# Kernel optimization log

Measured on AMD Instinct MI355X. Metric: run time of the kernel, lower is better.

Reference implementation:

```python
import jax, jax.numpy as jnp
import numpy as np
from jax import lax

FH, FW = 38, 63          # feature map H,W (600x1000 image, stride 16)
A = 9                    # anchors per location (3 scales x 3 ratios)
POOL = 7                 # cfg.POOLING_SIZE
PRE_NMS, POST_NMS = 6000, 300
NMS_THRESH = 0.7
IM_H, IM_W = 600.0, 1000.0
STRIDE = 16.0


def _make_anchors(h, w, stride=16):
    ratios = np.array([0.5, 1.0, 2.0]); scales = np.array([8.0, 16.0, 32.0])
    base = 16.0; ctr = (base - 1.0) / 2.0
    ws = np.round(np.sqrt(base * base / ratios)); hs = np.round(ws * ratios)
    ws = (ws[:, None] * scales[None, :]).ravel(); hs = (hs[:, None] * scales[None, :]).ravel()
    ba = np.stack([ctr - 0.5 * (ws - 1), ctr - 0.5 * (hs - 1),
                   ctr + 0.5 * (ws - 1), ctr + 0.5 * (hs - 1)], 1)
    sx, sy = np.meshgrid(np.arange(w) * stride, np.arange(h) * stride)
    shifts = np.stack([sx.ravel(), sy.ravel(), sx.ravel(), sy.ravel()], 1)
    return (shifts[:, None, :] + ba[None]).reshape(-1, 4).astype(np.float32)


def _conv(x, w, b, pad):
    y = lax.conv_general_dilated(x, w, (1, 1), pad,
                                 dimension_numbers=('NCHW', 'OIHW', 'NCHW'))
    return y + b[None, :, None, None]


def _bbox_transform_inv(anchors, deltas):
    w = anchors[:, 2] - anchors[:, 0] + 1.0
    h = anchors[:, 3] - anchors[:, 1] + 1.0
    cx = anchors[:, 0] + 0.5 * w
    cy = anchors[:, 1] + 0.5 * h
    dx, dy, dw, dh = deltas[:, 0], deltas[:, 1], deltas[:, 2], deltas[:, 3]
    pcx = dx * w + cx; pcy = dy * h + cy
    pw = jnp.exp(dw) * w; ph = jnp.exp(dh) * h
    return jnp.stack([pcx - 0.5 * pw, pcy - 0.5 * ph,
                      pcx + 0.5 * pw, pcy + 0.5 * ph], 1)


def _nms_keep(boxes, thresh):
    # greedy NMS over score-sorted boxes, fixed-size keep mask
    x1, y1, x2, y2 = boxes[:, 0], boxes[:, 1], boxes[:, 2], boxes[:, 3]
    areas = (x2 - x1 + 1.0) * (y2 - y1 + 1.0)
    iw = jnp.maximum(jnp.minimum(x2[:, None], x2[None, :])
                     - jnp.maximum(x1[:, None], x1[None, :]) + 1.0, 0.0)
    ih = jnp.maximum(jnp.minimum(y2[:, None], y2[None, :])
                     - jnp.maximum(y1[:, None], y1[None, :]) + 1.0, 0.0)
    inter = iw * ih
    iou = inter / (areas[:, None] + areas[None, :] - inter)
    n = boxes.shape[0]; ar = jnp.arange(n)
    def body(i, keep):
        sup = (iou[i] > thresh) & (ar > i) & keep[i]
        return keep & ~sup
    return lax.fori_loop(0, n, body, jnp.ones((n,), bool))


def _crop_and_resize(feat, boxes, crop):
    # feat [C,H,W]; boxes [R,4] normalized (y1,x1,y2,x2); TF crop_and_resize semantics
    C, H, W = feat.shape
    t = jnp.arange(crop, dtype=feat.dtype) / (crop - 1)
    def one(box):
        by1, bx1, by2, bx2 = box
        ys = by1 * (H - 1) + t * (by2 - by1) * (H - 1)
        xs = bx1 * (W - 1) + t * (bx2 - bx1) * (W - 1)
        y0f = jnp.floor(ys); x0f = jnp.floor(xs)
        wy = (ys - y0f)[None, :, None]; wx = (xs - x0f)[None, None, :]
        y0 = jnp.clip(y0f, 0, H - 1).astype(jnp.int32)
        y1i = jnp.clip(y0f + 1, 0, H - 1).astype(jnp.int32)
        x0 = jnp.clip(x0f, 0, W - 1).astype(jnp.int32)
        x1i = jnp.clip(x0f + 1, 0, W - 1).astype(jnp.int32)
        f00 = feat[:, y0][:, :, x0]; f01 = feat[:, y0][:, :, x1i]
        f10 = feat[:, y1i][:, :, x0]; f11 = feat[:, y1i][:, :, x1i]
        return (f00 * (1 - wy) * (1 - wx) + f01 * (1 - wy) * wx
                + f10 * wy * (1 - wx) + f11 * wy * wx)
    return jax.vmap(one)(boxes)


def _forward(net_conv, w_rpn, b_rpn, w_cls, b_cls, w_bbox, b_bbox, anchors):
    # _region_proposal: 3x3 rpn conv + relu, 1x1 cls / bbox heads
    rpn = jax.nn.relu(_conv(net_conv, w_rpn, b_rpn, 'SAME'))
    cls = _conv(rpn, w_cls, b_cls, 'VALID')    # [1,2A,H,W]
    bbox = _conv(rpn, w_bbox, b_bbox, 'VALID')  # [1,4A,H,W]
    # view(1,2,-1,W) softmax: channel a pairs with channel a+A (bg/fg)
    bg, fg = cls[:, :A], cls[:, A:]
    fg_prob = jax.nn.softmax(jnp.stack([bg, fg], axis=1), axis=1)[:, 1]  # [1,A,H,W]
    scores = jnp.transpose(fg_prob, (0, 2, 3, 1)).reshape(-1)            # (H*W*A,)
    deltas = jnp.transpose(bbox, (0, 2, 3, 1)).reshape(-1, 4)
    proposals = _bbox_transform_inv(anchors, deltas)
    proposals = jnp.stack([jnp.clip(proposals[:, 0], 0.0, IM_W - 1.0),
                           jnp.clip(proposals[:, 1], 0.0, IM_H - 1.0),
                           jnp.clip(proposals[:, 2], 0.0, IM_W - 1.0),
                           jnp.clip(proposals[:, 3], 0.0, IM_H - 1.0)], 1)
    # proposal selection is non-differentiable (rois.detach() in original)
    scores_sg = lax.stop_gradient(scores)
    props_sg = lax.stop_gradient(proposals)
    _, order = lax.top_k(scores_sg, PRE_NMS)
    boxes = props_sg[order]
    keep = _nms_keep(boxes, NMS_THRESH)
    idx = jnp.sort(jnp.where(keep, jnp.arange(PRE_NMS), PRE_NMS))[:POST_NMS]
    rois = boxes[jnp.minimum(idx, PRE_NMS - 1)]  # [300,4] (x1,y1,x2,y2)
    # _crop_pool_layer with max_pool=True: crop to 14x14 then 2x2 max pool
    H, W = net_conv.shape[2], net_conv.shape[3]
    x1 = rois[:, 0] / STRIDE; y1 = rois[:, 1] / STRIDE
    x2 = rois[:, 2] / STRIDE; y2 = rois[:, 3] / STRIDE
    norm = jnp.stack([y1 / (H - 1), x1 / (W - 1), y2 / (H - 1), x2 / (W - 1)], 1)
    crops = _crop_and_resize(net_conv[0], norm, 2 * POOL)  # [300,C,14,14]
    R, C = crops.shape[0], crops.shape[1]
    return crops.reshape(R, C, POOL, 2, POOL, 2).max(axis=(3, 5))  # [300,C,7,7]


def setup_inputs():
    key = jax.random.key(0)
    ks = jax.random.split(key, 4)
    net_conv = jax.random.normal(ks[0], (1, 512, FH, FW), jnp.float32)
    w_rpn = jax.random.normal(ks[1], (512, 512, 3, 3), jnp.float32) * 0.01
    b_rpn = jnp.zeros((512,), jnp.float32)
    w_cls = jax.random.normal(ks[2], (2 * A, 512, 1, 1), jnp.float32) * 0.01
    b_cls = jnp.zeros((2 * A,), jnp.float32)
    w_bbox = jax.random.normal(ks[3], (4 * A, 512, 1, 1), jnp.float32) * 0.01
    b_bbox = jnp.zeros((4 * A,), jnp.float32)
    anchors = jnp.asarray(_make_anchors(FH, FW))
    return {"net_conv": net_conv, "w_rpn": w_rpn, "b_rpn": b_rpn,
            "w_cls": w_cls, "b_cls": b_cls, "w_bbox": w_bbox,
            "b_bbox": b_bbox, "anchors": anchors}


def reference(net_conv, w_rpn, b_rpn, w_cls, b_cls, w_bbox, b_bbox, anchors):
    return _forward(net_conv, w_rpn, b_rpn, w_cls, b_cls, w_bbox, b_bbox, anchors)
```

## Files before the change

kernel.cpp:

```cpp
#include <hip/hip_runtime.h>
#include <stdint.h>

#define NPOS 2394
#define CIN 512
#define KK 4608
#define NANCH 21546
#define PRE 6000
#define POST 300
#define NWORD 94
#define NQ 8
#define QLEN 2694
#define FEATT_BYTES 4902912

#define OFF_BH    0
#define OFF_BL    4718592
#define OFF_P0    9437184
#define OFF_SBOX  9437184
#define OFF_KEEP  9533440
#define OFF_DIAG  9633792
#define OFF_P1    14340096
#define OFF_KEYS  19243008
#define OFF_PROP  19415552
#define OFF_RPART 19760384
#define OFF_FPH   20450048
#define OFF_FPL   23179264

typedef _Float16 half8 __attribute__((ext_vector_type(8)));
typedef float f32x4 __attribute__((ext_vector_type(4)));

__device__ __forceinline__ void gload16(const void* g, void* l) {
    __builtin_amdgcn_global_load_lds((const __attribute__((address_space(1))) void*)g,
                                     (__attribute__((address_space(3))) void*)l, 16, 0, 0);
}

__device__ __forceinline__ unsigned long long rl64(unsigned long long v, int l) {
    union { unsigned long long q; unsigned int d[2]; } s; s.q = v;
    unsigned int lo = __builtin_amdgcn_readlane(s.d[0], l);
    unsigned int hi = __builtin_amdgcn_readlane(s.d[1], l);
    return ((unsigned long long)hi << 32) | (unsigned long long)lo;
}

__global__ __launch_bounds__(256) void k_transpose_feat(const float* __restrict__ in,
                                                        float* __restrict__ featT) {
    __shared__ float tl[32][33];
    int tx = threadIdx.x & 31, tg = threadIdx.x >> 5;
    int posBase = blockIdx.x * 32, ciBase = blockIdx.y * 32;
#pragma unroll
    for (int j = 0; j < 4; ++j) {
        int ci = ciBase + tg + j * 8;
        int pos = posBase + tx;
        tl[tg + j * 8][tx] = (pos < NPOS) ? in[(size_t)ci * NPOS + pos] : 0.f;
    }
    __syncthreads();
#pragma unroll
    for (int j = 0; j < 4; ++j) {
        int pos = posBase + tg + j * 8;
        int ci = ciBase + tx;
        if (pos < NPOS) featT[(size_t)pos * 512 + ci] = tl[tx][tg + j * 8];
    }
}

__global__ void k_pad_split(const float* __restrict__ featT,
                            _Float16* __restrict__ FPH, _Float16* __restrict__ FPL) {
    int idx = blockIdx.x * 256 + threadIdx.x;
    int ci = idx & 511;
    int rc = idx >> 9;
    int hp = rc / 65, wp = rc - hp * 65;
    int h = hp - 1, w = wp - 1;
    float a = 0.f;
    if ((unsigned)h < 38u && (unsigned)w < 63u)
        a = featT[(size_t)(h * 63 + w) * 512 + ci] * 16.f;
    _Float16 ah = (_Float16)a;
    _Float16 al = (_Float16)(a - (float)ah);
    FPH[idx] = ah; FPL[idx] = al;
}

__global__ void k_prep_wf16(const float* __restrict__ w,
                            _Float16* __restrict__ BH, _Float16* __restrict__ BL) {
    int idx = blockIdx.x * 256 + threadIdx.x;
    int co = idx / KK;
    int rem = idx - co * KK;
    int p = rem >> 9;
    int ci = rem & 511;
    float b = w[(co * CIN + ci) * 9 + p] * 128.f;
    _Float16 bh = (_Float16)b;
    _Float16 bl = (_Float16)(b - (float)bh);
    BH[idx] = bh; BL[idx] = bl;
}

__global__ __launch_bounds__(256, 3) void k_conv3_mfma(
    const _Float16* __restrict__ FPH, const _Float16* __restrict__ FPL,
    const _Float16* __restrict__ BHp, const _Float16* __restrict__ BLp,
    float* __restrict__ P0, float* __restrict__ P1)
{
    __shared__ __align__(16) char lds[49152];
    const int t = threadIdx.x;
    const int wave = t >> 6, lane = t & 63;
    const int posBase = blockIdx.x * 128;
    const int coBase  = blockIdx.y * 64;
    const int z = blockIdx.z;
    float* __restrict__ P = z ? P1 : P0;
    const int wm = wave >> 1, wn = wave & 1;
    const int lr = lane & 15, lg = lane >> 4;

    int addrA[4][2], addrB[2][2];
#pragma unroll
    for (int m = 0; m < 4; ++m) {
        int row = wm * 64 + m * 16 + lr;
        int x = row & 7;
        addrA[m][0] = row * 128 + ((lg ^ x) << 4);
        addrA[m][1] = row * 128 + (((4 + lg) ^ x) << 4);
    }
#pragma unroll
    for (int n = 0; n < 2; ++n) {
        int row = wn * 32 + n * 16 + lr;
        int x = row & 7;
        addrB[n][0] = 32768 + row * 128 + ((lg ^ x) << 4);
        addrB[n][1] = 32768 + row * 128 + (((4 + lg) ^ x) << 4);
    }

    int baseA[4], ldsAo[4];
#pragma unroll
    for (int s = 0; s < 4; ++s) {
        int row = (wave * 4 + s) * 8 + (lane >> 3);
        int pos = posBase + row;
        int h = pos / 63;
        int w = pos - h * 63;
        int swz = ((lane & 7) ^ (row & 7)) * 8;
        baseA[s] = (h * 65 + w) * 512 + swz;
        ldsAo[s] = (wave * 4 + s) * 1024 + lane * 16;
    }
    int baseB[2], ldsBo[2];
#pragma unroll
    for (int s = 0; s < 2; ++s) {
        int row = (wave * 2 + s) * 8 + (lane >> 3);
        int swz = ((lane & 7) ^ (row & 7)) * 8;
        baseB[s] = (coBase + row) * KK + swz;
        ldsBo[s] = 32768 + (wave * 2 + s) * 1024 + lane * 16;
    }

    f32x4 acc[4][2];
#pragma unroll
    for (int m = 0; m < 4; ++m)
#pragma unroll
        for (int n = 0; n < 2; ++n) acc[m][n] = (f32x4){0.f, 0.f, 0.f, 0.f};

    const int kbeg = z * 2304;
    for (int step = 0; step < 36; ++step) {
        int k0 = kbeg + step * 64;
        int p = k0 >> 9;
        int ci0 = k0 & 511;
        int kh = p / 3;
        int kw = p - kh * 3;
        int dA = (kh * 65 + kw) * 512 + ci0;
#pragma unroll
        for (int s = 0; s < 4; ++s) {
            int so = baseA[s] + dA;
            gload16(FPH + so, lds + ldsAo[s]);
            gload16(FPL + so, lds + 16384 + ldsAo[s]);
        }
#pragma unroll
        for (int s = 0; s < 2; ++s) {
            int so = baseB[s] + k0;
            gload16(BHp + so, lds + ldsBo[s]);
            gload16(BLp + so, lds + 8192 + ldsBo[s]);
        }
        __syncthreads();
#pragma unroll
        for (int ks = 0; ks < 2; ++ks) {
            half8 aH[4], aL[4], bH[2], bL[2];
#pragma unroll
            for (int m = 0; m < 4; ++m) {
                aH[m] = *(const half8*)(lds + addrA[m][ks]);
                aL[m] = *(const half8*)(lds + 16384 + addrA[m][ks]);
            }
#pragma unroll
            for (int n = 0; n < 2; ++n) {
                bH[n] = *(const half8*)(lds + addrB[n][ks]);
                bL[n] = *(const half8*)(lds + 8192 + addrB[n][ks]);
            }
#pragma unroll
            for (int m = 0; m < 4; ++m)
#pragma unroll
                for (int n = 0; n < 2; ++n) {
                    acc[m][n] = __builtin_amdgcn_mfma_f32_16x16x32_f16(aH[m], bH[n], acc[m][n], 0, 0, 0);
                    acc[m][n] = __builtin_amdgcn_mfma_f32_16x16x32_f16(aH[m], bL[n], acc[m][n], 0, 0, 0);
                    acc[m][n] = __builtin_amdgcn_mfma_f32_16x16x32_f16(aL[m], bH[n], acc[m][n], 0, 0, 0);
                }
        }
        __syncthreads();
    }

#pragma unroll
    for (int m = 0; m < 4; ++m) {
        int pbase = posBase + wm * 64 + m * 16 + lg * 4;
        int co = coBase + wn * 32 + lr;
#pragma unroll
        for (int r = 0; r < 4; ++r) {
            int pos = pbase + r;
            if (pos < NPOS) {
                P[(size_t)pos * 512 + co]      = acc[m][0][r] * (1.f / 2048.f);
                P[(size_t)pos * 512 + co + 16] = acc[m][1][r] * (1.f / 2048.f);
            }
        }
    }
}

__global__ __launch_bounds__(256) void k_heads(const float* __restrict__ P0,
                                               const float* __restrict__ P1,
                                               const float* __restrict__ brpn,
                                               const float* __restrict__ wcls,
                                               const float* __restrict__ bcls,
                                               const float* __restrict__ wbbox,
                                               const float* __restrict__ bbbox,
                                               const float* __restrict__ anchors,
                                               float* __restrict__ proposals,
                                               unsigned long long* __restrict__ keys) {
    __shared__ float x[512];
    __shared__ float part[54][4];
    __shared__ float logit[54];
    int pos = blockIdx.x;
    int t = threadIdx.x;
    {
        float v0 = P0[(size_t)pos * 512 + t] + P1[(size_t)pos * 512 + t] + brpn[t];
        float v1 = P0[(size_t)pos * 512 + t + 256] + P1[(size_t)pos * 512 + t + 256] + brpn[t + 256];
        x[t] = v0 > 0.f ? v0 : 0.f;
        x[t + 256] = v1 > 0.f ? v1 : 0.f;
    }
    __syncthreads();
    if (t < 216) {
        int o = t >> 2, q = t & 3;
        const float* wr = (o < 18) ? (wcls + o * 512) : (wbbox + (o - 18) * 512);
        float s = 0.f;
        int base = q * 128;
#pragma unroll 4
        for (int k2 = 0; k2 < 128; ++k2) s += x[base + k2] * wr[base + k2];
        part[o][q] = s;
    }
    __syncthreads();
    if (t < 54) {
        float b = (t < 18) ? bcls[t] : bbbox[t - 18];
        logit[t] = part[t][0] + part[t][1] + part[t][2] + part[t][3] + b;
    }
    __syncthreads();
    if (t < 9) {
        int a = t;
        float bg = logit[a], fg = logit[9 + a];
        float score = 1.f / (1.f + expf(bg - fg));
        float dx = logit[18 + 4 * a], dy = logit[19 + 4 * a];
        float dw = logit[20 + 4 * a], dh = logit[21 + 4 * a];
        int idx = pos * 9 + a;
        float ax1 = anchors[idx * 4 + 0], ay1 = anchors[idx * 4 + 1];
        float ax2 = anchors[idx * 4 + 2], ay2 = anchors[idx * 4 + 3];
        float aw = ax2 - ax1 + 1.f, ah = ay2 - ay1 + 1.f;
        float cx = ax1 + 0.5f * aw, cy = ay1 + 0.5f * ah;
        float pcx = dx * aw + cx, pcy = dy * ah + cy;
        float pw = expf(dw) * aw, ph = expf(dh) * ah;
        float x1 = fminf(fmaxf(pcx - 0.5f * pw, 0.f), 999.f);
        float y1 = fminf(fmaxf(pcy - 0.5f * ph, 0.f), 599.f);
        float x2 = fminf(fmaxf(pcx + 0.5f * pw, 0.f), 999.f);
        float y2 = fminf(fmaxf(pcy + 0.5f * ph, 0.f), 599.f);
        proposals[idx * 4 + 0] = x1; proposals[idx * 4 + 1] = y1;
        proposals[idx * 4 + 2] = x2; proposals[idx * 4 + 3] = y2;
        union { float f; unsigned int i; } sv; sv.f = score;
        keys[idx] = (((unsigned long long)sv.i) << 32) |
                    (unsigned long long)(0xFFFFFFFFu - (unsigned)idx);
    }
}

__global__ __launch_bounds__(256) void k_rank_partial(const unsigned long long* __restrict__ keys,
                                                      unsigned int* __restrict__ rpart) {
    __shared__ unsigned long long kc[1024];
    int i = blockIdx.x * 256 + threadIdx.x;
    int q = blockIdx.y;
    unsigned long long myk = (i < NANCH) ? keys[i] : 0xFFFFFFFFFFFFFFFFull;
    int j0 = q * QLEN;
    int j1 = j0 + QLEN; if (j1 > NANCH) j1 = NANCH;
    unsigned int cnt = 0;
    for (int base = j0; base < j1; base += 1024) {
        int nload = j1 - base; if (nload > 1024) nload = 1024;
        __syncthreads();
        for (int u = threadIdx.x; u < 1024; u += 256)
            kc[u] = (base + u < j1) ? keys[base + u] : 0ull;
        __syncthreads();
        for (int u = 0; u < nload; ++u)
            cnt += (kc[u] > myk) ? 1u : 0u;
    }
    if (i < NANCH) rpart[i * NQ + q] = cnt;
}

__global__ void k_zero_sboxes(float* __restrict__ sboxes) {
    int i = blockIdx.x * 256 + threadIdx.x;
    if (i < PRE * 4) sboxes[i] = 0.f;
}

__global__ void k_rank_scatter(const unsigned int* __restrict__ rpart,
                               const float* __restrict__ proposals,
                               float* __restrict__ sboxes) {
    int i = blockIdx.x * 256 + threadIdx.x;
    if (i >= NANCH) return;
    unsigned int r = 0;
#pragma unroll
    for (int q = 0; q < NQ; q++) r += rpart[i * NQ + q];
    if (r < PRE) {
        sboxes[r * 4 + 0] = proposals[i * 4 + 0];
        sboxes[r * 4 + 1] = proposals[i * 4 + 1];
        sboxes[r * 4 + 2] = proposals[i * 4 + 2];
        sboxes[r * 4 + 3] = proposals[i * 4 + 3];
    }
}

__global__ __launch_bounds__(64) void k_nms_mask(const float* __restrict__ sboxes,
                                                 unsigned long long* __restrict__ mask,
                                                 unsigned long long* __restrict__ diag2) {
    __shared__ float bx[64][4];
    int ib = blockIdx.x, jb = blockIdx.y;
    int lane = threadIdx.x;
    int j = jb * 64 + lane;
    if (j < PRE) {
        bx[lane][0] = sboxes[j * 4 + 0]; bx[lane][1] = sboxes[j * 4 + 1];
        bx[lane][2] = sboxes[j * 4 + 2]; bx[lane][3] = sboxes[j * 4 + 3];
    } else {
        bx[lane][0] = 3e8f; bx[lane][1] = 3e8f; bx[lane][2] = 3e8f; bx[lane][3] = 3e8f;
    }
    __syncthreads();
    int i = ib * 64 + lane;
    if (i >= PRE) return;
    float x1 = sboxes[i * 4 + 0], y1 = sboxes[i * 4 + 1];
    float x2 = sboxes[i * 4 + 2], y2 = sboxes[i * 4 + 3];
    float ar = (x2 - x1 + 1.f) * (y2 - y1 + 1.f);
    unsigned long long bits = 0;
#pragma unroll 4
    for (int u = 0; u < 64; u++) {
        int j2 = jb * 64 + u;
        float iw = fminf(x2, bx[u][2]) - fmaxf(x1, bx[u][0]) + 1.f;
        float ih = fminf(y2, bx[u][3]) - fmaxf(y1, bx[u][1]) + 1.f;
        iw = fmaxf(iw, 0.f); ih = fmaxf(ih, 0.f);
        float inter = iw * ih;
        float arj = (bx[u][2] - bx[u][0] + 1.f) * (bx[u][3] - bx[u][1] + 1.f);
        float iou = inter / (ar + arj - inter);
        if (iou > 0.7f && j2 > i) bits |= (1ull << u);
    }
    mask[(size_t)i * NWORD + jb] = bits;
    if ((ib >> 1) == (jb >> 1)) diag2[(size_t)i * 2 + (jb & 1)] = bits;
}

#define NSLOT 12
__global__ __launch_bounds__(64) void k_nms_scan(const unsigned long long* __restrict__ mask,
                                                 const unsigned long long* __restrict__ diag2,
                                                 int* __restrict__ keep) {
    __shared__ __align__(16) unsigned long long ldsd[12032];
    __shared__ __align__(16) char ldsrow[NSLOT * 1024];
    __shared__ int ldsk[POST];
    const int lane = threadIdx.x;

    {
        const char* g = (const char*)diag2;
        char* l = (char*)ldsd;
        for (int r = 0; r < 94; ++r)
            gload16(g + (size_t)r * 1024 + (size_t)lane * 16, l + r * 1024);
        asm volatile("s_waitcnt vmcnt(0)" ::: "memory");
        __builtin_amdgcn_sched_barrier(0);
    }

    unsigned long long rem0 = 0, rem1 = 0;
    int nk = 0;
    int npend = 0;

    for (int sb = 0; sb < 47; ++sb) {
        if (npend) {
            asm volatile("s_waitcnt vmcnt(0)" ::: "memory");
            __builtin_amdgcn_sched_barrier(0);
            for (int q = 0; q < npend; ++q) {
                const unsigned long long* lr = (const unsigned long long*)(ldsrow + q * 1024);
                rem0 |= lr[lane];
                if (lane < NWORD - 64) rem1 |= lr[64 + lane];
            }
            npend = 0;
        }
        const int w0 = 2 * sb;
        const int base = sb * 128;
        ulonglong2 lo = *reinterpret_cast<const ulonglong2*>(&ldsd[(size_t)(base + lane) * 2]);
        unsigned long long c1b = ldsd[(size_t)(base + 64 + lane) * 2 + 1];

        unsigned long long rm0 = (w0 < 64) ? rl64(rem0, w0) : rl64(rem1, w0 - 64);
        unsigned long long rm1 = (w0 + 1 < 64) ? rl64(rem0, w0 + 1) : rl64(rem1, w0 + 1 - 64);
        const unsigned long long valid1 = (sb == 46) ? ((1ull << 48) - 1) : ~0ull;
        unsigned long long above0 = ~0ull, above1 = ~0ull;

        for (;;) {
            unsigned long long a0 = ~rm0 & above0;
            if (a0) {
                int u = (int)(__ffsll((long long)a0) - 1);
                if (npend == NSLOT) {
                    asm volatile("s_waitcnt vmcnt(0)" ::: "memory");
                    __builtin_amdgcn_sched_barrier(0);
                    for (int q = 0; q < NSLOT; ++q) {
                        const unsigned long long* lr = (const unsigned long long*)(ldsrow + q * 1024);
                        rem0 |= lr[lane];
                        if (lane < NWORD - 64) rem1 |= lr[64 + lane];
                    }
                    npend = 0;
                }
                gload16((const char*)(mask + (size_t)(base + u) * NWORD) + (size_t)lane * 16,
                        ldsrow + npend * 1024);
                ++npend;
                if (lane == 0) ldsk[nk] = base + u;
                ++nk; if (nk == POST) goto done;
                rm0 |= rl64(lo.x, u);
                rm1 |= rl64(lo.y, u);
                above0 = (u == 63) ? 0ull : (~0ull << (u + 1));
                continue;
            }
            unsigned long long a1 = ~rm1 & valid1 & above1;
            if (a1) {
                int u = (int)(__ffsll((long long)a1) - 1);
                if (npend == NSLOT) {
                    asm volatile("s_waitcnt vmcnt(0)" ::: "memory");
                    __builtin_amdgcn_sched_barrier(0);
                    for (int q = 0; q < NSLOT; ++q) {
                        const unsigned long long* lr = (const unsigned long long*)(ldsrow + q * 1024);
                        rem0 |= lr[lane];
                        if (lane < NWORD - 64) rem1 |= lr[64 + lane];
                    }
                    npend = 0;
                }
                gload16((const char*)(mask + (size_t)(base + 64 + u) * NWORD) + (size_t)lane * 16,
                        ldsrow + npend * 1024);
                ++npend;
                if (lane == 0) ldsk[nk] = base + 64 + u;
                ++nk; if (nk == POST) goto done;
                rm1 |= rl64(c1b, u);
                above1 = (u == 63) ? 0ull : (~0ull << (u + 1));
                continue;
            }
            break;
        }
    }
done:
    asm volatile("s_waitcnt vmcnt(0)" ::: "memory");
    for (int k2 = lane; k2 < POST; k2 += 64)
        keep[k2] = (k2 < nk) ? ldsk[k2] : PRE - 1;
}

__global__ __launch_bounds__(256) void k_gather_rois(const float* sboxes, const int* keep,
                                                     float* outF) {
    int t = threadIdx.x;
    float4 box[2];
    int nr = 0;
    for (int r = t; r < POST; r += 256) {
        int ki = keep[r];
        if (ki < 0) ki = 0; if (ki > PRE - 1) ki = PRE - 1;
        box[nr++] = *reinterpret_cast<const float4*>(sboxes + ki * 4);
    }
    __syncthreads();
    nr = 0;
    for (int r = t; r < POST; r += 256) {
        float4 b = box[nr++];
#pragma unroll
        for (int cg = 0; cg < 8; ++cg)
            *reinterpret_cast<float4*>(outF + (size_t)(r * 512 + cg * 64) * 49) = b;
    }
}

__global__ __launch_bounds__(256) void k_crop_fast(const float* __restrict__ featT,
                                                   float* out) {
    __shared__ float lds[4][49 * 65];
    int r = blockIdx.x;
    int w = threadIdx.x >> 6, lane = threadIdx.x & 63;
    int cg = blockIdx.y * 4 + w;
    int c = cg * 64 + lane;
    float* chunk = out + (size_t)(r * 512 + cg * 64) * 49;
    const float4 b = *reinterpret_cast<const float4*>(chunk);
    float x1 = b.x, y1 = b.y, x2 = b.z, y2 = b.w;
    float by1 = (y1 / 16.f) / 37.f, bx1 = (x1 / 16.f) / 62.f;
    float by2 = (y2 / 16.f) / 37.f, bx2 = (x2 / 16.f) / 62.f;
    float dyn = by2 - by1, dxn = bx2 - bx1;
    for (int e = 0; e < 49; ++e) {
        int oy = e / 7, ox = e - oy * 7;
        float vv[4];
#pragma unroll
        for (int dy = 0; dy < 2; ++dy) {
            int sy = 2 * oy + dy;
            float ty = (float)sy / 13.f;
            float ys = by1 * 37.f + (ty * dyn) * 37.f;
            float yf = floorf(ys);
            float wy = ys - yf;
            int y0  = (int)fminf(fmaxf(yf, 0.f), 37.f);
            int y1i = (int)fminf(fmaxf(yf + 1.f, 0.f), 37.f);
#pragma unroll
            for (int dxx = 0; dxx < 2; ++dxx) {
                int sx = 2 * ox + dxx;
                float tx = (float)sx / 13.f;
                float xs = bx1 * 62.f + (tx * dxn) * 62.f;
                float xf = floorf(xs);
                float wx = xs - xf;
                int x0  = (int)fminf(fmaxf(xf, 0.f), 62.f);
                int x1i = (int)fminf(fmaxf(xf + 1.f, 0.f), 62.f);
                float f00 = featT[(size_t)(y0 * 63 + x0) * 512 + c];
                float f01 = featT[(size_t)(y0 * 63 + x1i) * 512 + c];
                float f10 = featT[(size_t)(y1i * 63 + x0) * 512 + c];
                float f11 = featT[(size_t)(y1i * 63 + x1i) * 512 + c];
                vv[dy * 2 + dxx] = f00 * (1.f - wy) * (1.f - wx) + f01 * (1.f - wy) * wx +
                                   f10 * wy * (1.f - wx) + f11 * wy * wx;
            }
        }
        lds[w][e * 65 + lane] = fmaxf(fmaxf(vv[0], vv[1]), fmaxf(vv[2], vv[3]));
    }
    __syncthreads();
    for (int i = lane; i < 64 * 49; i += 64) {
        int cl = i / 49, e = i - cl * 49;
        chunk[i] = lds[w][e * 65 + cl];
    }
}

__global__ __launch_bounds__(64) void k_crop_slow(const float* __restrict__ net,
                                                  float* out) {
    int r = blockIdx.x, cg = blockIdx.y;
    int lane = threadIdx.x;
    int c = cg * 64 + lane;
    const float4 b = *reinterpret_cast<const float4*>(out + (size_t)(r * 512 + cg * 64) * 49);
    float x1 = b.x, y1 = b.y, x2 = b.z, y2 = b.w;
    float by1 = (y1 / 16.f) / 37.f, bx1 = (x1 / 16.f) / 62.f;
    float by2 = (y2 / 16.f) / 37.f, bx2 = (x2 / 16.f) / 62.f;
    float dyn = by2 - by1, dxn = bx2 - bx1;
    const float* fc = net + (size_t)c * NPOS;
    float* orow = out + ((size_t)r * 512 + c) * 49;
    for (int e = 0; e < 49; ++e) {
        int oy = e / 7, ox = e - oy * 7;
        float vv[4];
#pragma unroll
        for (int dy = 0; dy < 2; ++dy) {
            int sy = 2 * oy + dy;
            float ty = (float)sy / 13.f;
            float ys = by1 * 37.f + (ty * dyn) * 37.f;
            float yf = floorf(ys);
            float wy = ys - yf;
            int y0  = (int)fminf(fmaxf(yf, 0.f), 37.f);
            int y1i = (int)fminf(fmaxf(yf + 1.f, 0.f), 37.f);
#pragma unroll
            for (int dxx = 0; dxx < 2; ++dxx) {
                int sx = 2 * ox + dxx;
                float tx = (float)sx / 13.f;
                float xs = bx1 * 62.f + (tx * dxn) * 62.f;
                float xf = floorf(xs);
                float wx = xs - xf;
                int x0  = (int)fminf(fmaxf(xf, 0.f), 62.f);
                int x1i = (int)fminf(fmaxf(xf + 1.f, 0.f), 62.f);
                float f00 = fc[y0 * 63 + x0];
                float f01 = fc[y0 * 63 + x1i];
                float f10 = fc[y1i * 63 + x0];
                float f11 = fc[y1i * 63 + x1i];
                vv[dy * 2 + dxx] = f00 * (1.f - wy) * (1.f - wx) + f01 * (1.f - wy) * wx +
                                   f10 * wy * (1.f - wx) + f11 * wy * wx;
            }
        }
        orow[e] = fmaxf(fmaxf(vv[0], vv[1]), fmaxf(vv[2], vv[3]));
    }
}

extern "C" void kernel_launch(void* const* d_in, const int* in_sizes, int n_in,
                              void* d_out, int out_size, void* d_ws, size_t ws_size,
                              hipStream_t stream) {
    auto find = [&](int count, int fallback) {
        for (int i = 0; i < n_in; ++i) if (in_sizes[i] == count) return i;
        return fallback;
    };
    const float* net   = (const float*)d_in[find(NPOS * CIN, 0)];
    const float* wrpn  = (const float*)d_in[find(512 * KK, 1)];
    const float* brpn  = (const float*)d_in[find(512, 2)];
    const float* wcls  = (const float*)d_in[find(18 * 512, 3)];
    const float* bcls  = (const float*)d_in[find(18, 4)];
    const float* wbbox = (const float*)d_in[find(36 * 512, 5)];
    const float* bbbox = (const float*)d_in[find(36, 6)];
    const float* anch  = (const float*)d_in[find(NANCH * 4, 7)];

    char* ob = (char*)d_out;
    _Float16* BH             = (_Float16*)(ob + OFF_BH);
    _Float16* BL             = (_Float16*)(ob + OFF_BL);
    unsigned long long* mask = (unsigned long long*)(ob + OFF_BH);
    float* P0                = (float*)(ob + OFF_P0);
    float* P1                = (float*)(ob + OFF_P1);
    float* sboxes            = (float*)(ob + OFF_SBOX);
    int* keep                = (int*)(ob + OFF_KEEP);
    unsigned long long* diag2= (unsigned long long*)(ob + OFF_DIAG);
    unsigned long long* keys = (unsigned long long*)(ob + OFF_KEYS);
    float* proposals         = (float*)(ob + OFF_PROP);
    unsigned int* rpart      = (unsigned int*)(ob + OFF_RPART);
    _Float16* FPH            = (_Float16*)(ob + OFF_FPH);
    _Float16* FPL            = (_Float16*)(ob + OFF_FPL);
    float* outF              = (float*)d_out;

    const bool ws_ok = (ws_size >= (size_t)FEATT_BYTES);
    float* featT = ws_ok ? (float*)d_ws : (float*)(ob + OFF_P0);

    hipLaunchKernelGGL(k_transpose_feat, dim3(75, 16), dim3(256), 0, stream, net, featT);
    hipLaunchKernelGGL(k_pad_split, dim3(5330), dim3(256), 0, stream, featT, FPH, FPL);
    hipLaunchKernelGGL(k_prep_wf16, dim3(9216), dim3(256), 0, stream, wrpn, BH, BL);
    hipLaunchKernelGGL(k_conv3_mfma, dim3(19, 8, 2), dim3(256), 0, stream, FPH, FPL, BH, BL, P0, P1);
    hipLaunchKernelGGL(k_heads, dim3(NPOS), dim3(256), 0, stream, P0, P1, brpn, wcls, bcls, wbbox, bbbox, anch, proposals, keys);
    hipLaunchKernelGGL(k_rank_partial, dim3(85, NQ), dim3(256), 0, stream, keys, rpart);
    hipLaunchKernelGGL(k_zero_sboxes, dim3((PRE * 4 + 255) / 256), dim3(256), 0, stream, sboxes);
    hipLaunchKernelGGL(k_rank_scatter, dim3(85), dim3(256), 0, stream, rpart, proposals, sboxes);
    hipLaunchKernelGGL(k_nms_mask, dim3(NWORD, NWORD), dim3(64), 0, stream, sboxes, mask, diag2);
    hipLaunchKernelGGL(k_nms_scan, dim3(1), dim3(64), 0, stream, mask, diag2, keep);
    hipLaunchKernelGGL(k_gather_rois, dim3(1), dim3(256), 0, stream, sboxes, keep, outF);
    if (ws_ok)
        hipLaunchKernelGGL(k_crop_fast, dim3(POST, 2), dim3(256), 0, stream, featT, outF);
    else
        hipLaunchKernelGGL(k_crop_slow, dim3(POST, 8), dim3(64), 0, stream, net, outF);
}
```

Before: 414.7 us.

## Widen NMS scan super-blocks to 256 boxes with double-buffered diagonal tiles

```diff
diff --git a/kernel.cpp b/kernel.cpp
--- a/kernel.cpp
+++ b/kernel.cpp
@@ -289,8 +289,9 @@
     if (i < NANCH) rpart[i * NQ + q] = cnt;
 }
 
-__global__ void k_zero_sboxes(float* __restrict__ sboxes) {
+__global__ void k_zero_aux(float* __restrict__ sboxes, unsigned long long* __restrict__ diag4) {
     int i = blockIdx.x * 256 + threadIdx.x;
+    diag4[i] = 0ull;
     if (i < PRE * 4) sboxes[i] = 0.f;
 }
 
@@ -312,7 +313,7 @@
 
 __global__ __launch_bounds__(64) void k_nms_mask(const float* __restrict__ sboxes,
                                                  unsigned long long* __restrict__ mask,
-                                                 unsigned long long* __restrict__ diag2) {
+                                                 unsigned long long* __restrict__ diag4) {
     __shared__ float bx[64][4];
     int ib = blockIdx.x, jb = blockIdx.y;
     int lane = threadIdx.x;
@@ -342,56 +343,89 @@
         if (iou > 0.7f && j2 > i) bits |= (1ull << u);
     }
     mask[(size_t)i * NWORD + jb] = bits;
-    if ((ib >> 1) == (jb >> 1)) diag2[(size_t)i * 2 + (jb & 1)] = bits;
-}
-
-#define NSLOT 12
+    if ((jb >> 2) == (ib >> 2)) diag4[(size_t)i * 4 + (jb & 3)] = bits;
+}
+
+#define NSB 24
+#define SBW 256
+#define NSLOT 20
 __global__ __launch_bounds__(64) void k_nms_scan(const unsigned long long* __restrict__ mask,
-                                                 const unsigned long long* __restrict__ diag2,
+                                                 const unsigned long long* __restrict__ diag4,
                                                  int* __restrict__ keep) {
-    __shared__ __align__(16) unsigned long long ldsd[12032];
+    __shared__ __align__(16) unsigned long long tile[2][SBW * 4];
     __shared__ __align__(16) char ldsrow[NSLOT * 1024];
     __shared__ int ldsk[POST];
     const int lane = threadIdx.x;
-
-    {
-        const char* g = (const char*)diag2;
-        char* l = (char*)ldsd;
-        for (int r = 0; r < 94; ++r)
-            gload16(g + (size_t)r * 1024 + (size_t)lane * 16, l + r * 1024);
-        asm volatile("s_waitcnt vmcnt(0)" ::: "memory");
+    const char* dg = (const char*)diag4;
+
+    for (int c = 0; c < 8; ++c)
+        gload16(dg + c * 1024 + (size_t)lane * 16, (char*)tile[0] + c * 1024);
+
+    unsigned long long rem0 = 0, rem1 = 0;
+    int nk = 0, npend = 0;
+
+    for (int sb = 0; sb < NSB; ++sb) {
+        if (sb + 1 < NSB) {
+            const char* src = dg + (size_t)(sb + 1) * 8192;
+            char* dst = (char*)tile[(sb + 1) & 1];
+            for (int c = 0; c < 8; ++c)
+                gload16(src + c * 1024 + (size_t)lane * 16, dst + c * 1024);
+            asm volatile("s_waitcnt vmcnt(8)" ::: "memory");
+        } else {
+            asm volatile("s_waitcnt vmcnt(0)" ::: "memory");
+        }
         __builtin_amdgcn_sched_barrier(0);
-    }
-
-    unsigned long long rem0 = 0, rem1 = 0;
-    int nk = 0;
-    int npend = 0;
-
-    for (int sb = 0; sb < 47; ++sb) {
-        if (npend) {
-            asm volatile("s_waitcnt vmcnt(0)" ::: "memory");
-            __builtin_amdgcn_sched_barrier(0);
-            for (int q = 0; q < npend; ++q) {
-                const unsigned long long* lr = (const unsigned long long*)(ldsrow + q * 1024);
-                rem0 |= lr[lane];
-                if (lane < NWORD - 64) rem1 |= lr[64 + lane];
+
+        for (int q = 0; q < npend; ++q) {
+            const unsigned long long* lr = (const unsigned long long*)(ldsrow + q * 1024);
+            rem0 |= lr[lane];
+            if (lane < NWORD - 64) rem1 |= lr[64 + lane];
+        }
+        npend = 0;
+
+        const unsigned long long* tl = tile[sb & 1];
+        unsigned long long d[4][4];
+#pragma unroll
+        for (int q = 0; q < 4; ++q) {
+            ulonglong2 e0 = *(const ulonglong2*)&tl[(q * 64 + lane) * 4];
+            ulonglong2 e1 = *(const ulonglong2*)&tl[(q * 64 + lane) * 4 + 2];
+            d[q][0] = e0.x; d[q][1] = e0.y; d[q][2] = e1.x; d[q][3] = e1.y;
+        }
+
+        const int w0 = 4 * sb;
+        const int base = sb * SBW;
+        unsigned long long rmw[4];
+#pragma unroll
+        for (int j = 0; j < 4; ++j) {
+            int w = w0 + j;
+            rmw[j] = (w < 64) ? rl64(rem0, w) : ((w < NWORD) ? rl64(rem1, w - 64) : ~0ull);
+        }
+
+#pragma unroll
+        for (int p = 0; p < 4; ++p) {
+            int w = w0 + p;
+            if (w >= NWORD) break;
+            const unsigned long long valid = (w == NWORD - 1) ? ((1ull << 48) - 1) : ~0ull;
+            unsigned long long above = ~0ull;
+            unsigned long long keptm = 0;
+            for (;;) {
+                unsigned long long a = ~rmw[p] & valid & above;
+                if (!a) break;
+                int u = (int)(__ffsll((long long)a) - 1);
+                keptm |= 1ull << u;
+                ++nk;
+#pragma unroll
+                for (int j = p; j < 4; ++j) rmw[j] |= rl64(d[p][j], u);
+                if (nk == POST) break;
+                above = (u == 63) ? 0ull : (~0ull << (u + 1));
             }
-            npend = 0;
-        }
-        const int w0 = 2 * sb;
-        const int base = sb * 128;
-        ulonglong2 lo = *reinterpret_cast<const ulonglong2*>(&ldsd[(size_t)(base + lane) * 2]);
-        unsigned long long c1b = ldsd[(size_t)(base + 64 + lane) * 2 + 1];
-
-        unsigned long long rm0 = (w0 < 64) ? rl64(rem0, w0) : rl64(rem1, w0 - 64);
-        unsigned long long rm1 = (w0 + 1 < 64) ? rl64(rem0, w0 + 1) : rl64(rem1, w0 + 1 - 64);
-        const unsigned long long valid1 = (sb == 46) ? ((1ull << 48) - 1) : ~0ull;
-        unsigned long long above0 = ~0ull, above1 = ~0ull;
-
-        for (;;) {
-            unsigned long long a0 = ~rm0 & above0;
-            if (a0) {
-                int u = (int)(__ffsll((long long)a0) - 1);
+            unsigned long long bits = keptm;
+            int nkb = nk - __builtin_popcountll(keptm);
+            while (bits) {
+                int u = (int)(__ffsll((long long)bits) - 1); bits &= bits - 1;
+                int i = base + p * 64 + u;
+                if (lane == 0) ldsk[nkb] = i;
+                ++nkb;
                 if (npend == NSLOT) {
                     asm volatile("s_waitcnt vmcnt(0)" ::: "memory");
                     __builtin_amdgcn_sched_barrier(0);
@@ -402,39 +436,11 @@
                     }
                     npend = 0;
                 }
-                gload16((const char*)(mask + (size_t)(base + u) * NWORD) + (size_t)lane * 16,
+                gload16((const char*)(mask + (size_t)i * NWORD) + (size_t)lane * 16,
                         ldsrow + npend * 1024);
                 ++npend;
-                if (lane == 0) ldsk[nk] = base + u;
-                ++nk; if (nk == POST) goto done;
-                rm0 |= rl64(lo.x, u);
-                rm1 |= rl64(lo.y, u);
-                above0 = (u == 63) ? 0ull : (~0ull << (u + 1));
-                continue;
             }
-            unsigned long long a1 = ~rm1 & valid1 & above1;
-            if (a1) {
-                int u = (int)(__ffsll((long long)a1) - 1);
-                if (npend == NSLOT) {
-                    asm volatile("s_waitcnt vmcnt(0)" ::: "memory");
-                    __builtin_amdgcn_sched_barrier(0);
-                    for (int q = 0; q < NSLOT; ++q) {
-                        const unsigned long long* lr = (const unsigned long long*)(ldsrow + q * 1024);
-                        rem0 |= lr[lane];
-                        if (lane < NWORD - 64) rem1 |= lr[64 + lane];
-                    }
-                    npend = 0;
-                }
-                gload16((const char*)(mask + (size_t)(base + 64 + u) * NWORD) + (size_t)lane * 16,
-                        ldsrow + npend * 1024);
-                ++npend;
-                if (lane == 0) ldsk[nk] = base + 64 + u;
-                ++nk; if (nk == POST) goto done;
-                rm1 |= rl64(c1b, u);
-                above1 = (u == 63) ? 0ull : (~0ull << (u + 1));
-                continue;
-            }
-            break;
+            if (nk >= POST) goto done;
         }
     }
 done:
@@ -583,7 +589,7 @@
     float* P1                = (float*)(ob + OFF_P1);
     float* sboxes            = (float*)(ob + OFF_SBOX);
     int* keep                = (int*)(ob + OFF_KEEP);
-    unsigned long long* diag2= (unsigned long long*)(ob + OFF_DIAG);
+    unsigned long long* diag4= (unsigned long long*)(ob + OFF_DIAG);
     unsigned long long* keys = (unsigned long long*)(ob + OFF_KEYS);
     float* proposals         = (float*)(ob + OFF_PROP);
     unsigned int* rpart      = (unsigned int*)(ob + OFF_RPART);
@@ -600,10 +606,10 @@
     hipLaunchKernelGGL(k_conv3_mfma, dim3(19, 8, 2), dim3(256), 0, stream, FPH, FPL, BH, BL, P0, P1);
     hipLaunchKernelGGL(k_heads, dim3(NPOS), dim3(256), 0, stream, P0, P1, brpn, wcls, bcls, wbbox, bbbox, anch, proposals, keys);
     hipLaunchKernelGGL(k_rank_partial, dim3(85, NQ), dim3(256), 0, stream, keys, rpart);
-    hipLaunchKernelGGL(k_zero_sboxes, dim3((PRE * 4 + 255) / 256), dim3(256), 0, stream, sboxes);
+    hipLaunchKernelGGL(k_zero_aux, dim3(96), dim3(256), 0, stream, sboxes, diag4);
     hipLaunchKernelGGL(k_rank_scatter, dim3(85), dim3(256), 0, stream, rpart, proposals, sboxes);
-    hipLaunchKernelGGL(k_nms_mask, dim3(NWORD, NWORD), dim3(64), 0, stream, sboxes, mask, diag2);
-    hipLaunchKernelGGL(k_nms_scan, dim3(1), dim3(64), 0, stream, mask, diag2, keep);
+    hipLaunchKernelGGL(k_nms_mask, dim3(NWORD, NWORD), dim3(64), 0, stream, sboxes, mask, diag4);
+    hipLaunchKernelGGL(k_nms_scan, dim3(1), dim3(64), 0, stream, mask, diag4, keep);
     hipLaunchKernelGGL(k_gather_rois, dim3(1), dim3(256), 0, stream, sboxes, keep, outF);
     if (ws_ok)
         hipLaunchKernelGGL(k_crop_fast, dim3(POST, 2), dim3(256), 0, stream, featT, outF);
```

New measurement: 410.5 us. No clear change (-1.0%).
